# Performance work log

Measured on AMD Instinct MI355X. Metric: run time of the kernel, lower is better.

Reference implementation:

```python
import jax, jax.numpy as jnp
import numpy as np

IN_FEATURES = 1024
OUT_FEATURES = 1024
THRESHOLD = 0.05


def ternary_quantize(x, threshold):
    # {-1, 0, +1}: zero where |x| < threshold, else sign(x)
    return jnp.where(jnp.abs(x) < threshold, jnp.zeros_like(x), jnp.sign(x))


def setup_inputs() -> dict:
    key = jax.random.key(0)
    kx, kw = jax.random.split(key)
    x = jax.random.normal(kx, (32768, IN_FEATURES), dtype=jnp.float32)
    # xavier_uniform for weight [out, in]: bound = sqrt(6/(fan_in+fan_out))
    bound = float(np.sqrt(6.0 / (IN_FEATURES + OUT_FEATURES)))
    weight = jax.random.uniform(kw, (OUT_FEATURES, IN_FEATURES), dtype=jnp.float32,
                                minval=-bound, maxval=bound)
    return {"x": x, "weight": weight}


def reference(x, weight):
    x_tern = ternary_quantize(x, THRESHOLD).astype(jnp.int8)
    w_tern = ternary_quantize(weight, THRESHOLD).astype(jnp.int8)
    # int32 accumulate matmul: [T, in] @ [in, out] -> [T, out]
    out = jnp.matmul(x_tern.astype(jnp.int32), w_tern.astype(jnp.int32).T)
    return out.astype(jnp.float32)
```

## Files before the change

kernel.cpp:

```cpp
#include <hip/hip_runtime.h>

#define THRESH 0.05f

typedef __attribute__((ext_vector_type(4)))  int   int32x4;
typedef __attribute__((ext_vector_type(16))) int   int32x16;
typedef __attribute__((ext_vector_type(4)))  float floatx4;

__global__ __launch_bounds__(256) void quant_w_kernel(const float* __restrict__ w,
                                                      signed char* __restrict__ wqf) {
    int c = blockIdx.x * 256 + threadIdx.x;
    int l  = c & 63;
    int k  = (c >> 6) & 31;
    int nb = c >> 11;
    int col   = nb * 32 + (l & 31);
    int kbase = k * 32 + (l >> 5) * 16;
    const float* src = w + col * 1024 + kbase;
    signed char q[16];
    #pragma unroll
    for (int j = 0; j < 4; ++j) {
        float4 f = *(const float4*)(src + j * 4);
        q[j * 4 + 0] = (signed char)((f.x >= THRESH) - (f.x <= -THRESH));
        q[j * 4 + 1] = (signed char)((f.y >= THRESH) - (f.y <= -THRESH));
        q[j * 4 + 2] = (signed char)((f.z >= THRESH) - (f.z <= -THRESH));
        q[j * 4 + 3] = (signed char)((f.w >= THRESH) - (f.w <= -THRESH));
    }
    *(int32x4*)(wqf + (size_t)c * 16) = *(const int32x4*)q;
}

__global__ __launch_bounds__(256, 4) void tern_gemm_kernel(const float* __restrict__ x,
                                                           const signed char* __restrict__ wqf,
                                                           float* __restrict__ out) {
    __shared__ __attribute__((aligned(16))) signed char a_lds[32 * 1024];
    const int tid = threadIdx.x;
    const long rowbase = (long)blockIdx.x * 32;

    #pragma unroll
    for (int i = 0; i < 8; ++i) {
        int c   = tid + i * 256;
        int row = c >> 6;
        int cir = c & 63;
        const floatx4* src = (const floatx4*)(x + (rowbase + row) * 1024 + cir * 16);
        signed char q[16];
        #pragma unroll
        for (int j = 0; j < 4; ++j) {
            floatx4 f = __builtin_nontemporal_load(src + j);
            #pragma unroll
            for (int e = 0; e < 4; ++e)
                q[j * 4 + e] = (signed char)((f[e] >= THRESH) - (f[e] <= -THRESH));
        }
        int swz = (cir ^ (row & 7)) * 16;
        *(int32x4*)(a_lds + row * 1024 + swz) = *(const int32x4*)q;
    }
    __syncthreads();

    const int wave  = tid >> 6;
    const int lane  = tid & 63;
    const int l31   = lane & 31;
    const int hi    = lane >> 5;
    const int ex    = l31 & 7;
    const int abase = l31 * 1024;

    for (int ot = 0; ot < 4; ++ot) {
        const int nb0 = ot * 8 + wave * 2;
        const signed char* bp = wqf + (size_t)nb0 * 32768 + lane * 16;

        int32x16 acc0 = {0,0,0,0,0,0,0,0,0,0,0,0,0,0,0,0};
        int32x16 acc1 = {0,0,0,0,0,0,0,0,0,0,0,0,0,0,0,0};

        #pragma unroll
        for (int ks = 0; ks < 8; ++ks) {
            int32x4 b0[4], b1[4];
            #pragma unroll
            for (int j = 0; j < 4; ++j) {
                b0[j] = *(const int32x4*)(bp + (size_t)(ks * 4 + j) * 1024);
                b1[j] = *(const int32x4*)(bp + 32768 + (size_t)(ks * 4 + j) * 1024);
            }
            __builtin_amdgcn_sched_barrier(0);
            #pragma unroll
            for (int j = 0; j < 4; ++j) {
                int k2 = (ks * 4 + j) * 2 + hi;
                int32x4 af = *(const int32x4*)(a_lds + abase + ((k2 ^ ex) * 16));
                acc0 = __builtin_amdgcn_mfma_i32_32x32x32_i8(af, b0[j], acc0, 0, 0, 0);
                acc1 = __builtin_amdgcn_mfma_i32_32x32x32_i8(af, b1[j], acc1, 0, 0, 0);
            }
        }

        const int cb = ot * 256 + wave * 64 + l31;
        #pragma unroll
        for (int r = 0; r < 16; ++r) {
            int row = (r & 3) + 8 * (r >> 2) + 4 * hi;
            float* o = out + (rowbase + row) * 1024 + cb;
            __builtin_nontemporal_store((float)acc0[r], o);
            __builtin_nontemporal_store((float)acc1[r], o + 32);
        }
    }
}

extern "C" void kernel_launch(void* const* d_in, const int* in_sizes, int n_in,
                              void* d_out, int out_size, void* d_ws, size_t ws_size,
                              hipStream_t stream) {
    const float* x = (const float*)d_in[0];
    const float* w = (const float*)d_in[1];
    float* out = (float*)d_out;
    signed char* wqf = (signed char*)d_ws;

    quant_w_kernel<<<dim3(256), dim3(256), 0, stream>>>(w, wqf);
    tern_gemm_kernel<<<dim3(1024), dim3(256), 0, stream>>>(x, wqf, out);
}
```

Baseline: 276.9 us.

## Double row tile to 64 with 512 threads, 2x2 MFMA per wave, prefetch B

Each block now quantizes 64 rows of x into a re-laid-out, swizzled LDS buffer and runs 8 waves. Each wave computes a 2x2 grid of 32x32 MFMA tiles, so every B fragment loaded from global memory is reused across two A fragments, halving weight reads per output. B loads are software-prefetched one k-group ahead instead of being fenced by a sched barrier. LDS use doubles to 64KB and accumulator registers double, which may reduce occupancy.

```diff
diff --git a/kernel.cpp b/kernel.cpp
--- a/kernel.cpp
+++ b/kernel.cpp
@@ -27,16 +27,16 @@
     *(int32x4*)(wqf + (size_t)c * 16) = *(const int32x4*)q;
 }
 
-__global__ __launch_bounds__(256, 4) void tern_gemm_kernel(const float* __restrict__ x,
+__global__ __launch_bounds__(512, 4) void tern_gemm_kernel(const float* __restrict__ x,
                                                            const signed char* __restrict__ wqf,
                                                            float* __restrict__ out) {
-    __shared__ __attribute__((aligned(16))) signed char a_lds[32 * 1024];
+    __shared__ __attribute__((aligned(16))) signed char a_lds[64 * 1024];
     const int tid = threadIdx.x;
-    const long rowbase = (long)blockIdx.x * 32;
+    const long rowbase = (long)blockIdx.x * 64;
 
     #pragma unroll
     for (int i = 0; i < 8; ++i) {
-        int c   = tid + i * 256;
+        int c   = tid + i * 512;
         int row = c >> 6;
         int cir = c & 63;
         const floatx4* src = (const floatx4*)(x + (rowbase + row) * 1024 + cir * 16);
@@ -48,50 +48,72 @@
             for (int e = 0; e < 4; ++e)
                 q[j * 4 + e] = (signed char)((f[e] >= THRESH) - (f[e] <= -THRESH));
         }
-        int swz = (cir ^ (row & 7)) * 16;
-        *(int32x4*)(a_lds + row * 1024 + swz) = *(const int32x4*)q;
+        int k    = cir >> 1;
+        int blk  = k * 2 + (row >> 5);
+        int slot = ((cir & 1) * 32 + (row & 31)) ^ (k & 7);
+        *(int32x4*)(a_lds + blk * 1024 + slot * 16) = *(const int32x4*)q;
     }
     __syncthreads();
 
-    const int wave  = tid >> 6;
-    const int lane  = tid & 63;
-    const int l31   = lane & 31;
-    const int hi    = lane >> 5;
-    const int ex    = l31 & 7;
-    const int abase = l31 * 1024;
+    const int wave = tid >> 6;
+    const int lane = tid & 63;
+    const int l31  = lane & 31;
+    const int hi   = lane >> 5;
 
-    for (int ot = 0; ot < 4; ++ot) {
-        const int nb0 = ot * 8 + wave * 2;
-        const signed char* bp = wqf + (size_t)nb0 * 32768 + lane * 16;
+    for (int ot = 0; ot < 2; ++ot) {
+        const int nb0 = ot * 16 + wave * 2;
+        const signed char* bp0 = wqf + (size_t)nb0 * 32768 + lane * 16;
+        const signed char* bp1 = bp0 + 32768;
 
-        int32x16 acc0 = {0,0,0,0,0,0,0,0,0,0,0,0,0,0,0,0};
-        int32x16 acc1 = {0,0,0,0,0,0,0,0,0,0,0,0,0,0,0,0};
+        int32x16 acc00 = {0,0,0,0,0,0,0,0,0,0,0,0,0,0,0,0};
+        int32x16 acc01 = acc00;
+        int32x16 acc10 = acc00;
+        int32x16 acc11 = acc00;
 
+        int32x4 b0[4], b1[4];
         #pragma unroll
-        for (int ks = 0; ks < 8; ++ks) {
-            int32x4 b0[4], b1[4];
+        for (int j = 0; j < 4; ++j) {
+            b0[j] = *(const int32x4*)(bp0 + (size_t)j * 1024);
+            b1[j] = *(const int32x4*)(bp1 + (size_t)j * 1024);
+        }
+
+        for (int kk = 0; kk < 28; kk += 4) {
             #pragma unroll
             for (int j = 0; j < 4; ++j) {
-                b0[j] = *(const int32x4*)(bp + (size_t)(ks * 4 + j) * 1024);
-                b1[j] = *(const int32x4*)(bp + 32768 + (size_t)(ks * 4 + j) * 1024);
-            }
-            __builtin_amdgcn_sched_barrier(0);
-            #pragma unroll
-            for (int j = 0; j < 4; ++j) {
-                int k2 = (ks * 4 + j) * 2 + hi;
-                int32x4 af = *(const int32x4*)(a_lds + abase + ((k2 ^ ex) * 16));
-                acc0 = __builtin_amdgcn_mfma_i32_32x32x32_i8(af, b0[j], acc0, 0, 0, 0);
-                acc1 = __builtin_amdgcn_mfma_i32_32x32x32_i8(af, b1[j], acc1, 0, 0, 0);
+                const int k  = kk + j;
+                const int sl = ((lane ^ (k & 7)) * 16);
+                int32x4 af0 = *(const int32x4*)(a_lds + (k * 2 + 0) * 1024 + sl);
+                int32x4 af1 = *(const int32x4*)(a_lds + (k * 2 + 1) * 1024 + sl);
+                acc00 = __builtin_amdgcn_mfma_i32_32x32x32_i8(af0, b0[j], acc00, 0, 0, 0);
+                acc01 = __builtin_amdgcn_mfma_i32_32x32x32_i8(af0, b1[j], acc01, 0, 0, 0);
+                acc10 = __builtin_amdgcn_mfma_i32_32x32x32_i8(af1, b0[j], acc10, 0, 0, 0);
+                acc11 = __builtin_amdgcn_mfma_i32_32x32x32_i8(af1, b1[j], acc11, 0, 0, 0);
+                b0[j] = *(const int32x4*)(bp0 + (size_t)(k + 4) * 1024);
+                b1[j] = *(const int32x4*)(bp1 + (size_t)(k + 4) * 1024);
             }
         }
+        #pragma unroll
+        for (int j = 0; j < 4; ++j) {
+            const int k  = 28 + j;
+            const int sl = ((lane ^ (k & 7)) * 16);
+            int32x4 af0 = *(const int32x4*)(a_lds + (k * 2 + 0) * 1024 + sl);
+            int32x4 af1 = *(const int32x4*)(a_lds + (k * 2 + 1) * 1024 + sl);
+            acc00 = __builtin_amdgcn_mfma_i32_32x32x32_i8(af0, b0[j], acc00, 0, 0, 0);
+            acc01 = __builtin_amdgcn_mfma_i32_32x32x32_i8(af0, b1[j], acc01, 0, 0, 0);
+            acc10 = __builtin_amdgcn_mfma_i32_32x32x32_i8(af1, b0[j], acc10, 0, 0, 0);
+            acc11 = __builtin_amdgcn_mfma_i32_32x32x32_i8(af1, b1[j], acc11, 0, 0, 0);
+        }
 
-        const int cb = ot * 256 + wave * 64 + l31;
+        const int cb = nb0 * 32 + l31;
         #pragma unroll
         for (int r = 0; r < 16; ++r) {
-            int row = (r & 3) + 8 * (r >> 2) + 4 * hi;
-            float* o = out + (rowbase + row) * 1024 + cb;
-            __builtin_nontemporal_store((float)acc0[r], o);
-            __builtin_nontemporal_store((float)acc1[r], o + 32);
+            const int rit = (r & 3) + 8 * (r >> 2) + 4 * hi;
+            float* o0 = out + (rowbase + rit) * 1024 + cb;
+            float* o1 = o0 + 32L * 1024;
+            __builtin_nontemporal_store((float)acc00[r], o0);
+            __builtin_nontemporal_store((float)acc01[r], o0 + 32);
+            __builtin_nontemporal_store((float)acc10[r], o1);
+            __builtin_nontemporal_store((float)acc11[r], o1 + 32);
         }
     }
 }
@@ -105,5 +127,5 @@
     signed char* wqf = (signed char*)d_ws;
 
     quant_w_kernel<<<dim3(256), dim3(256), 0, stream>>>(w, wqf);
-    tern_gemm_kernel<<<dim3(1024), dim3(256), 0, stream>>>(x, wqf, out);
+    tern_gemm_kernel<<<dim3(512), dim3(512), 0, stream>>>(x, wqf, out);
 }
```

After: 431.3 us. +55.7%, slower.
